# Kernel optimization log

Hardware: AMD Instinct MI355X
Metric: run time of the kernel (lower is better)

The kernel has to match this reference:

```python
import jax, jax.numpy as jnp
import numpy as np

N = 50000
E = 1600000
IN_CH = 128
HID = 16
HEADS = 8
OUT_CH = 1
NEG_SLOPE = 0.2


def setup_inputs() -> dict:
    key = jax.random.key(0)
    ks = jax.random.split(key, 12)
    x = jax.random.normal(ks[0], (N, IN_CH), dtype=jnp.float32)
    edge_index = jax.random.randint(ks[1], (2, E), 0, N, dtype=jnp.int64)
    s1 = 1.0 / np.sqrt(IN_CH)
    s2 = 1.0 / np.sqrt(HEADS * HID)
    W1 = jax.random.normal(ks[2], (IN_CH, HEADS * HID), dtype=jnp.float32) * s1
    att_src1 = jax.random.normal(ks[3], (HEADS, HID), dtype=jnp.float32) * s1
    att_dst1 = jax.random.normal(ks[4], (HEADS, HID), dtype=jnp.float32) * s1
    b1 = jnp.zeros((HEADS * HID,), dtype=jnp.float32)
    W2 = jax.random.normal(ks[5], (HEADS * HID, OUT_CH), dtype=jnp.float32) * s2
    att_src2 = jax.random.normal(ks[6], (1, OUT_CH), dtype=jnp.float32) * s2
    att_dst2 = jax.random.normal(ks[7], (1, OUT_CH), dtype=jnp.float32) * s2
    b2 = jnp.zeros((OUT_CH,), dtype=jnp.float32)
    return {"x": x, "edge_index": edge_index,
            "W1": W1, "att_src1": att_src1, "att_dst1": att_dst1, "b1": b1,
            "W2": W2, "att_src2": att_src2, "att_dst2": att_dst2, "b2": b2}


def gat_conv(x, src, dst, W, att_src, att_dst, b, heads, concat):
    n = x.shape[0]
    h = (x @ W).reshape(n, heads, -1)               # [N, H, C]
    a_s = jnp.einsum('nhc,hc->nh', h, att_src)      # [N, H]
    a_d = jnp.einsum('nhc,hc->nh', h, att_dst)
    e = jax.nn.leaky_relu(a_s[src] + a_d[dst], NEG_SLOPE)  # [E, H]
    # segment softmax over incoming edges of each dst node
    emax = jax.ops.segment_max(e, dst, num_segments=n)
    p = jnp.exp(e - emax[dst])
    denom = jax.ops.segment_sum(p, dst, num_segments=n)
    alpha = p / (denom[dst] + 1e-16)                 # [E, H]
    msg = h[src] * alpha[:, :, None]                 # [E, H, C]
    out = jax.ops.segment_sum(msg, dst, num_segments=n)  # [N, H, C]
    if concat:
        out = out.reshape(n, -1)
    else:
        out = out.mean(axis=1)
    return out + b


def reference(x, edge_index, W1, att_src1, att_dst1, b1, W2, att_src2, att_dst2, b2):
    n = x.shape[0]
    loops = jnp.arange(n, dtype=edge_index.dtype)
    src = jnp.concatenate([edge_index[0], loops])    # PyG add_self_loops=True
    dst = jnp.concatenate([edge_index[1], loops])
    h = gat_conv(x, src, dst, W1, att_src1, att_dst1, b1, HEADS, True)
    h = jax.nn.elu(h)
    out = gat_conv(h, src, dst, W2, att_src2, att_dst2, b2, 1, False)
    return out
```

## Files before the change

kernel.cpp:

```cpp
#include <hip/hip_runtime.h>
#include <hip/hip_fp16.h>
#include <math.h>

#define N_NODES 50000
#define N_EDGES 1600000
#define NEG 0.2f

#define PB 256
#define CHUNK (N_EDGES / PB)
#define NC 196
#define S1 8960
#define BSHIFT 4
#define NBUCK (N_NODES >> BSHIFT)
#define STRIDE 768
#define GEMMB ((N_NODES + 31) / 32)


__global__ __launch_bounds__(256) void scatter_gemm(const int* __restrict__ ei, int* __restrict__ bcnt1,
                                                    int* __restrict__ temp1,
                                                    const float* __restrict__ x, const float* __restrict__ W1,
                                                    const float* __restrict__ att_s, const float* __restrict__ att_d,
                                                    __half2* __restrict__ h1, float* __restrict__ as1,
                                                    float* __restrict__ ad1) {
    __shared__ union {
        float xs[128][36];
        int cur[NC];
    } u;
    int t = threadIdx.x;
    if (blockIdx.x < PB) {
        int p = blockIdx.x;
        for (int i = t; i < NC; i += 256) u.cur[i] = 0;
        __syncthreads();
        int e0 = p * CHUNK;
        for (int e = e0 + t; e < e0 + CHUNK; e += 256) {
            int d = ei[N_EDGES + e];
            atomicAdd(&u.cur[d >> 8], 1);
        }
        __syncthreads();
        for (int i = t; i < NC; i += 256) {
            int h = u.cur[i];
            int c = i * S1;
            if (h) c += atomicAdd(&bcnt1[i], h);
            u.cur[i] = c;
        }
        __syncthreads();
        for (int e = e0 + t; e < e0 + CHUNK; e += 256) {
            int s = ei[e];
            int d = ei[N_EDGES + e];
            int b = d >> 8;
            int pos = atomicAdd(&u.cur[b], 1);
            if (pos < (b + 1) * S1)
                temp1[pos] = s | ((d & 255) << 16);
        }
        return;
    }
    int n0 = (blockIdx.x - PB) * 32;
#pragma unroll
    for (int i = 0; i < 16; ++i) {
        int f = i * 256 + t;
        int r = f >> 7, c = f & 127;
        int gr = n0 + r;
        float v = (gr < N_NODES) ? x[(size_t)gr * 128 + c] : 0.f;
        u.xs[c][r] = v;
    }
    __syncthreads();
    int c0 = (t & 31) * 4;
    int r0 = (t >> 5) * 4;
    float acc[4][4];
#pragma unroll
    for (int i = 0; i < 4; ++i)
#pragma unroll
        for (int j = 0; j < 4; ++j) acc[i][j] = 0.f;
#pragma unroll 4
    for (int k = 0; k < 128; ++k) {
        float4 w = *(const float4*)(W1 + k * 128 + c0);
        float4 xr = *(const float4*)(&u.xs[k][r0]);
        float xv[4] = {xr.x, xr.y, xr.z, xr.w};
        float wv[4] = {w.x, w.y, w.z, w.w};
#pragma unroll
        for (int i = 0; i < 4; ++i)
#pragma unroll
            for (int j = 0; j < 4; ++j) acc[i][j] += xv[i] * wv[j];
    }
#pragma unroll
    for (int i = 0; i < 4; ++i) {
        int row = n0 + r0 + i;
        if (row < N_NODES) {
            __half2 p0 = __float22half2_rn(make_float2(acc[i][0], acc[i][1]));
            __half2 p1 = __float22half2_rn(make_float2(acc[i][2], acc[i][3]));
            h1[(size_t)row * 64 + (c0 >> 1)] = p0;
            h1[(size_t)row * 64 + (c0 >> 1) + 1] = p1;
        }
    }
    int head = (t & 31) >> 2;
    float ps[4], pd[4];
#pragma unroll
    for (int i = 0; i < 4; ++i) {
        float s = 0.f, d = 0.f;
#pragma unroll
        for (int j = 0; j < 4; ++j) {
            s += acc[i][j] * att_s[c0 + j];
            d += acc[i][j] * att_d[c0 + j];
        }
        ps[i] = s; pd[i] = d;
    }
#pragma unroll
    for (int i = 0; i < 4; ++i) {
        ps[i] += __shfl_xor(ps[i], 1, 64);
        ps[i] += __shfl_xor(ps[i], 2, 64);
        pd[i] += __shfl_xor(pd[i], 1, 64);
        pd[i] += __shfl_xor(pd[i], 2, 64);
    }
    if ((t & 3) == 0) {
#pragma unroll
        for (int i = 0; i < 4; ++i) {
            int row = n0 + r0 + i;
            if (row < N_NODES) {
                as1[row * 8 + head] = ps[i];
                ad1[row * 8 + head] = pd[i];
            }
        }
    }
}


__global__ __launch_bounds__(256) void subsort(const int* __restrict__ temp1, const int* __restrict__ bcnt1,
                                               int* __restrict__ temp, int* __restrict__ bcnt) {
    __shared__ int cnt4[4][16];
    __shared__ int cur4[4][16];
    int cb = blockIdx.x, t = threadIdx.x;
    int wv = t >> 6;
    int base1 = cb * S1;
    int nE = min(bcnt1[cb], S1);
    if (t < 64) cnt4[t >> 4][t & 15] = 0;
    __syncthreads();
    for (int i = t; i < nE; i += 256) {
        int v = temp1[base1 + i];
        atomicAdd(&cnt4[wv][(v >> 20) & 15], 1);
    }
    __syncthreads();
    if (t < 16) {
        int c0 = cnt4[0][t], c1 = cnt4[1][t], c2 = cnt4[2][t], c3 = cnt4[3][t];
        int tot = c0 + c1 + c2 + c3;
        int gfb = cb * 16 + t;
        if (gfb < NBUCK) bcnt[gfb] = tot;
        int fbase = gfb * STRIDE;
        cur4[0][t] = fbase;
        cur4[1][t] = fbase + c0;
        cur4[2][t] = fbase + c0 + c1;
        cur4[3][t] = fbase + c0 + c1 + c2;
    }
    __syncthreads();
    for (int i = t; i < nE; i += 256) {
        int v = temp1[base1 + i];
        int fb = (v >> 20) & 15;
        int pos = atomicAdd(&cur4[wv][fb], 1);
        temp[pos] = (v & 0xFFFF) | (((v >> 16) & 15) << 16);
    }
}


__device__ __forceinline__ float lrelu(float v) { return fmaxf(v, NEG * v); }

__global__ __launch_bounds__(128) void agg1_kernel(const char* __restrict__ h1c, const char* __restrict__ as1c,
                                                   const float* __restrict__ ad1, const int* __restrict__ temp,
                                                   const int* __restrict__ bcnt, const float* __restrict__ b1,
                                                   const float* __restrict__ W2, float* __restrict__ h2out) {
    __shared__ int lsrc[STRIDE];
    __shared__ int cnt[16];
    __shared__ int cur[16];
    __shared__ int lrp[16];
    int b = blockIdx.x, t = threadIdx.x;
    int base = b * STRIDE;
    int nE = min(bcnt[b], STRIDE);
    if (t < 16) cnt[t] = 0;
    __syncthreads();
    for (int i = t; i < nE; i += 128)
        atomicAdd(&cnt[(unsigned)temp[base + i] >> 16], 1);
    __syncthreads();
    if (t < 16) {
        int v = cnt[t];
        int incl = v;
#pragma unroll
        for (int off = 1; off < 16; off <<= 1) {
            int u = __shfl_up(incl, off, 16);
            if (t >= off) incl += u;
        }
        int excl = incl - v;
        lrp[t] = excl;
        cur[t] = excl;
    }
    __syncthreads();
    for (int i = t; i < nE; i += 128) {
        int v = temp[base + i];
        int pos = atomicAdd(&cur[(unsigned)v >> 16], 1);
        lsrc[pos] = v & 0xFFFF;
    }
    __syncthreads();

    int lane = t & 63;
    int wave = t >> 6;
    int hB = lane >> 3;
    int hP = lane & 7;
    unsigned lane4 = (unsigned)lane << 2;
    unsigned hP4 = (unsigned)hP << 2;
    int bperm_base = hB << 2;
    int prod = lane >> 3;

    for (int kk = 0; kk < 8; ++kk) {
        int k = wave * 8 + kk;
        int n = b * 16 + k;

        float adP = ad1[n * 8 + hP];
        float adC = ad1[n * 8 + hB];
        float asC = *(const float*)(as1c + ((unsigned)n * 32u + ((unsigned)hB << 2)));
        float p_self = __expf(lrelu(asC + adC));
        __half2 hvs = *(const __half2*)(h1c + (((unsigned)n << 8) + lane4));
        float acc0 = p_self * __half2float(__low2half(hvs));
        float acc1 = p_self * __half2float(__high2half(hvs));
        float l = p_self;

        int jb = lrp[k];
        int deg = cnt[k];
        int j = 0;
        for (; j + 8 <= deg; j += 8) {
            int sP = lsrc[jb + j + prod];
            float aP = *(const float*)(as1c + (((unsigned)sP << 5) + hP4));
            float pP = __expf(lrelu(aP + adP));
            int pPi = __float_as_int(pP);
#pragma unroll
            for (int e = 0; e < 8; ++e) {
                int addr = bperm_base + e * 32;
                float p = __int_as_float(__builtin_amdgcn_ds_bpermute(addr, pPi));
                int s = __builtin_amdgcn_ds_bpermute(addr, sP);
                __half2 hv = *(const __half2*)(h1c + (((unsigned)s << 8) + lane4));
                acc0 += p * __half2float(__low2half(hv));
                acc1 += p * __half2float(__high2half(hv));
                l += p;
            }
        }
        if (j < deg) {
            int r = deg - j;
            int sP = 0;
            float pP = 0.f;
            if (j + prod < deg) {
                sP = lsrc[jb + j + prod];
                float aP = *(const float*)(as1c + (((unsigned)sP << 5) + hP4));
                pP = __expf(lrelu(aP + adP));
            }
            int pPi = __float_as_int(pP);
            for (int e = 0; e < r; ++e) {
                int addr = bperm_base + e * 32;
                float p = __int_as_float(__builtin_amdgcn_ds_bpermute(addr, pPi));
                int s = __builtin_amdgcn_ds_bpermute(addr, sP);
                __half2 hv = *(const __half2*)(h1c + (((unsigned)s << 8) + lane4));
                acc0 += p * __half2float(__low2half(hv));
                acc1 += p * __half2float(__high2half(hv));
                l += p;
            }
        }

        float inv = 1.f / (l + 1e-16f);
        int c0 = lane * 2;
        float y0 = acc0 * inv + b1[c0];
        float y1 = acc1 * inv + b1[c0 + 1];
        y0 = y0 > 0.f ? y0 : expm1f(y0);
        y1 = y1 > 0.f ? y1 : expm1f(y1);
        float part = y0 * W2[c0] + y1 * W2[c0 + 1];
#pragma unroll
        for (int off = 32; off; off >>= 1) part += __shfl_down(part, off, 64);
        if (lane == 0) h2out[n] = part;
    }
}


__global__ __launch_bounds__(128) void agg2_kernel(const float* __restrict__ h2, const int* __restrict__ temp,
                                                   const int* __restrict__ bcnt, const float* __restrict__ att_s2,
                                                   const float* __restrict__ att_d2, const float* __restrict__ b2,
                                                   float* __restrict__ out) {
    __shared__ int lsrc[STRIDE];
    __shared__ int cnt[16];
    __shared__ int cur[16];
    __shared__ int lrp[16];
    int b = blockIdx.x, t = threadIdx.x;
    int base = b * STRIDE;
    int nE = min(bcnt[b], STRIDE);
    if (t < 16) cnt[t] = 0;
    __syncthreads();
    for (int i = t; i < nE; i += 128)
        atomicAdd(&cnt[(unsigned)temp[base + i] >> 16], 1);
    __syncthreads();
    if (t < 16) {
        int v = cnt[t];
        int incl = v;
#pragma unroll
        for (int off = 1; off < 16; off <<= 1) {
            int u = __shfl_up(incl, off, 16);
            if (t >= off) incl += u;
        }
        int excl = incl - v;
        lrp[t] = excl;
        cur[t] = excl;
    }
    __syncthreads();
    for (int i = t; i < nE; i += 128) {
        int v = temp[base + i];
        int pos = atomicAdd(&cur[(unsigned)v >> 16], 1);
        lsrc[pos] = v & 0xFFFF;
    }
    __syncthreads();

    float asw = att_s2[0], adw = att_d2[0];
    int lane = t & 63;
    int wave = t >> 6;
    int sub = lane & 7;
    int k = wave * 8 + (lane >> 3);
    int n = b * 16 + k;
    float h2n = h2[n];
    float ad = h2n * adw;
    float acc = 0.f, l = 0.f;
    if (sub == 0) {
        float p = __expf(lrelu(h2n * asw + ad));
        acc = p * h2n;
        l = p;
    }
    int jb = lrp[k];
    int deg = cnt[k];
    for (int jj = sub; jj < deg; jj += 8) {
        int s = lsrc[jb + jj];
        float hs = h2[s];
        float p = __expf(lrelu(hs * asw + ad));
        acc += p * hs;
        l += p;
    }
#pragma unroll
    for (int off = 4; off; off >>= 1) {
        acc += __shfl_down(acc, off, 8);
        l += __shfl_down(l, off, 8);
    }
    if (sub == 0) out[n] = acc / (l + 1e-16f) + b2[0];
}


extern "C" void kernel_launch(void* const* d_in, const int* in_sizes, int n_in,
                              void* d_out, int out_size, void* d_ws, size_t ws_size,
                              hipStream_t stream) {
    const float* x = (const float*)d_in[0];
    const int* ei = (const int*)d_in[1];
    const float* W1 = (const float*)d_in[2];
    const float* att_s1 = (const float*)d_in[3];
    const float* att_d1 = (const float*)d_in[4];
    const float* b1 = (const float*)d_in[5];
    const float* W2 = (const float*)d_in[6];
    const float* att_s2 = (const float*)d_in[7];
    const float* att_d2 = (const float*)d_in[8];
    const float* b2 = (const float*)d_in[9];
    float* out = (float*)d_out;

    char* p = (char*)d_ws;
    auto alloc = [&](size_t bytes) {
        char* q = p;
        p += (bytes + 255) & ~(size_t)255;
        return q;
    };
    int* bcnt1 = (int*)alloc((size_t)NC * 4);
    int* bcnt = (int*)alloc((size_t)NBUCK * 4);
    int* temp1 = (int*)alloc((size_t)NC * S1 * 4);
    int* temp = (int*)alloc((size_t)NBUCK * STRIDE * 4);
    __half2* h1 = (__half2*)alloc((size_t)N_NODES * 128 * 2);
    float* as1 = (float*)alloc((size_t)N_NODES * 8 * 4);
    float* ad1 = (float*)alloc((size_t)N_NODES * 8 * 4);
    float* h2 = (float*)alloc((size_t)N_NODES * 4);

    hipMemsetAsync(bcnt1, 0, (size_t)NC * 4, stream);
    scatter_gemm<<<PB + GEMMB, 256, 0, stream>>>(ei, bcnt1, temp1,
                                                 x, W1, att_s1, att_d1, h1, as1, ad1);
    subsort<<<NC, 256, 0, stream>>>(temp1, bcnt1, temp, bcnt);
    agg1_kernel<<<NBUCK, 128, 0, stream>>>((const char*)h1, (const char*)as1, ad1, temp, bcnt, b1, W2, h2);
    agg2_kernel<<<NBUCK, 128, 0, stream>>>(h2, temp, bcnt, att_s2, att_d2, b2, out);
}
```

Measured before the change: 229.5 us.

## Fuse subsort into agg1 and pass compact 16-bit sources to agg2

Removes the separate subsort kernel. Each agg1 block instead filters its fine bucket directly from the coarse bucket array and builds its CSR in shared memory. agg1 also writes 16-bit source lists and per-node degrees, so agg2 can skip re-bucketing. This saves a launch and a global pass, but every block now scans the full coarse bucket twice, which is 16x redundant reads.

New measurement: 254.3 us. 10.8% more time.

```diff
diff --git a/kernel.cpp b/kernel.cpp
--- a/kernel.cpp
+++ b/kernel.cpp
@@ -10,8 +10,7 @@
 #define CHUNK (N_EDGES / PB)
 #define NC 196
 #define S1 8960
-#define BSHIFT 4
-#define NBUCK (N_NODES >> BSHIFT)
+#define NBUCK (N_NODES >> 4)
 #define STRIDE 768
 #define GEMMB ((N_NODES + 31) / 32)
 
@@ -124,59 +123,28 @@
 }
 
 
-__global__ __launch_bounds__(256) void subsort(const int* __restrict__ temp1, const int* __restrict__ bcnt1,
-                                               int* __restrict__ temp, int* __restrict__ bcnt) {
-    __shared__ int cnt4[4][16];
-    __shared__ int cur4[4][16];
-    int cb = blockIdx.x, t = threadIdx.x;
-    int wv = t >> 6;
-    int base1 = cb * S1;
-    int nE = min(bcnt1[cb], S1);
-    if (t < 64) cnt4[t >> 4][t & 15] = 0;
-    __syncthreads();
-    for (int i = t; i < nE; i += 256) {
-        int v = temp1[base1 + i];
-        atomicAdd(&cnt4[wv][(v >> 20) & 15], 1);
-    }
-    __syncthreads();
-    if (t < 16) {
-        int c0 = cnt4[0][t], c1 = cnt4[1][t], c2 = cnt4[2][t], c3 = cnt4[3][t];
-        int tot = c0 + c1 + c2 + c3;
-        int gfb = cb * 16 + t;
-        if (gfb < NBUCK) bcnt[gfb] = tot;
-        int fbase = gfb * STRIDE;
-        cur4[0][t] = fbase;
-        cur4[1][t] = fbase + c0;
-        cur4[2][t] = fbase + c0 + c1;
-        cur4[3][t] = fbase + c0 + c1 + c2;
-    }
-    __syncthreads();
-    for (int i = t; i < nE; i += 256) {
-        int v = temp1[base1 + i];
-        int fb = (v >> 20) & 15;
-        int pos = atomicAdd(&cur4[wv][fb], 1);
-        temp[pos] = (v & 0xFFFF) | (((v >> 16) & 15) << 16);
-    }
-}
-
-
 __device__ __forceinline__ float lrelu(float v) { return fmaxf(v, NEG * v); }
 
 __global__ __launch_bounds__(128) void agg1_kernel(const char* __restrict__ h1c, const char* __restrict__ as1c,
-                                                   const float* __restrict__ ad1, const int* __restrict__ temp,
-                                                   const int* __restrict__ bcnt, const float* __restrict__ b1,
-                                                   const float* __restrict__ W2, float* __restrict__ h2out) {
+                                                   const float* __restrict__ ad1, const int* __restrict__ temp1,
+                                                   const int* __restrict__ bcnt1, const float* __restrict__ b1,
+                                                   const float* __restrict__ W2, float* __restrict__ h2out,
+                                                   unsigned short* __restrict__ srcs16, int* __restrict__ ndeg) {
     __shared__ int lsrc[STRIDE];
     __shared__ int cnt[16];
     __shared__ int cur[16];
     __shared__ int lrp[16];
     int b = blockIdx.x, t = threadIdx.x;
-    int base = b * STRIDE;
-    int nE = min(bcnt[b], STRIDE);
+    int cb = b >> 4;
+    int f = b & 15;
+    int base1 = cb * S1;
+    int nE1 = min(bcnt1[cb], S1);
     if (t < 16) cnt[t] = 0;
     __syncthreads();
-    for (int i = t; i < nE; i += 128)
-        atomicAdd(&cnt[(unsigned)temp[base + i] >> 16], 1);
+    for (int i = t; i < nE1; i += 128) {
+        int v = temp1[base1 + i];
+        if (((v >> 20) & 15) == f) atomicAdd(&cnt[(v >> 16) & 15], 1);
+    }
     __syncthreads();
     if (t < 16) {
         int v = cnt[t];
@@ -189,14 +157,20 @@
         int excl = incl - v;
         lrp[t] = excl;
         cur[t] = excl;
-    }
-    __syncthreads();
-    for (int i = t; i < nE; i += 128) {
-        int v = temp[base + i];
-        int pos = atomicAdd(&cur[(unsigned)v >> 16], 1);
-        lsrc[pos] = v & 0xFFFF;
-    }
-    __syncthreads();
+        ndeg[b * 16 + t] = v;
+    }
+    __syncthreads();
+    for (int i = t; i < nE1; i += 128) {
+        int v = temp1[base1 + i];
+        if (((v >> 20) & 15) == f) {
+            int pos = atomicAdd(&cur[(v >> 16) & 15], 1);
+            if (pos < STRIDE) lsrc[pos] = v & 0xFFFF;
+        }
+    }
+    __syncthreads();
+    int nEf = min(lrp[15] + cnt[15], STRIDE);
+    for (int i = t; i < nEf; i += 128)
+        srcs16[(size_t)b * STRIDE + i] = (unsigned short)lsrc[i];
 
     int lane = t & 63;
     int wave = t >> 6;
@@ -274,40 +248,29 @@
 }
 
 
-__global__ __launch_bounds__(128) void agg2_kernel(const float* __restrict__ h2, const int* __restrict__ temp,
-                                                   const int* __restrict__ bcnt, const float* __restrict__ att_s2,
+__global__ __launch_bounds__(128) void agg2_kernel(const float* __restrict__ h2,
+                                                   const unsigned short* __restrict__ srcs16,
+                                                   const int* __restrict__ ndeg, const float* __restrict__ att_s2,
                                                    const float* __restrict__ att_d2, const float* __restrict__ b2,
                                                    float* __restrict__ out) {
     __shared__ int lsrc[STRIDE];
     __shared__ int cnt[16];
-    __shared__ int cur[16];
     __shared__ int lrp[16];
     int b = blockIdx.x, t = threadIdx.x;
-    int base = b * STRIDE;
-    int nE = min(bcnt[b], STRIDE);
-    if (t < 16) cnt[t] = 0;
-    __syncthreads();
-    for (int i = t; i < nE; i += 128)
-        atomicAdd(&cnt[(unsigned)temp[base + i] >> 16], 1);
-    __syncthreads();
     if (t < 16) {
-        int v = cnt[t];
+        int v = ndeg[b * 16 + t];
+        cnt[t] = v;
         int incl = v;
 #pragma unroll
         for (int off = 1; off < 16; off <<= 1) {
             int u = __shfl_up(incl, off, 16);
             if (t >= off) incl += u;
         }
-        int excl = incl - v;
-        lrp[t] = excl;
-        cur[t] = excl;
-    }
-    __syncthreads();
-    for (int i = t; i < nE; i += 128) {
-        int v = temp[base + i];
-        int pos = atomicAdd(&cur[(unsigned)v >> 16], 1);
-        lsrc[pos] = v & 0xFFFF;
-    }
+        lrp[t] = incl - v;
+    }
+    __syncthreads();
+    int nEf = min(lrp[15] + cnt[15], STRIDE);
+    for (int i = t; i < nEf; i += 128) lsrc[i] = srcs16[(size_t)b * STRIDE + i];
     __syncthreads();
 
     float asw = att_s2[0], adw = att_d2[0];
@@ -364,9 +327,9 @@
         return q;
     };
     int* bcnt1 = (int*)alloc((size_t)NC * 4);
-    int* bcnt = (int*)alloc((size_t)NBUCK * 4);
     int* temp1 = (int*)alloc((size_t)NC * S1 * 4);
-    int* temp = (int*)alloc((size_t)NBUCK * STRIDE * 4);
+    unsigned short* srcs16 = (unsigned short*)alloc((size_t)NBUCK * STRIDE * 2);
+    int* ndeg = (int*)alloc((size_t)NBUCK * 16 * 4);
     __half2* h1 = (__half2*)alloc((size_t)N_NODES * 128 * 2);
     float* as1 = (float*)alloc((size_t)N_NODES * 8 * 4);
     float* ad1 = (float*)alloc((size_t)N_NODES * 8 * 4);
@@ -375,7 +338,7 @@
     hipMemsetAsync(bcnt1, 0, (size_t)NC * 4, stream);
     scatter_gemm<<<PB + GEMMB, 256, 0, stream>>>(ei, bcnt1, temp1,
                                                  x, W1, att_s1, att_d1, h1, as1, ad1);
-    subsort<<<NC, 256, 0, stream>>>(temp1, bcnt1, temp, bcnt);
-    agg1_kernel<<<NBUCK, 128, 0, stream>>>((const char*)h1, (const char*)as1, ad1, temp, bcnt, b1, W2, h2);
-    agg2_kernel<<<NBUCK, 128, 0, stream>>>(h2, temp, bcnt, att_s2, att_d2, b2, out);
+    agg1_kernel<<<NBUCK, 128, 0, stream>>>((const char*)h1, (const char*)as1, ad1, temp1, bcnt1,
+                                           b1, W2, h2, srcs16, ndeg);
+    agg2_kernel<<<NBUCK, 128, 0, stream>>>(h2, srcs16, ndeg, att_s2, att_d2, b2, out);
 }
```
